# Kernel tuning notes

Measured on AMD Instinct MI355X. Metric: run time of the kernel, lower is better.

## Reference

```python
import jax, jax.numpy as jnp
import numpy as np

B, S, T = 16, 64, 64
H, V = 512, 32000


def _gru_step(h, x_t, W_ih, W_hh, b_ih, b_hh):
    # PyTorch GRU cell: gates ordered (r, z, n)
    gi = x_t @ W_ih.T + b_ih          # [B, 3H]
    gh = h @ W_hh.T + b_hh            # [B, 3H]
    i_r, i_z, i_n = jnp.split(gi, 3, axis=-1)
    h_r, h_z, h_n = jnp.split(gh, 3, axis=-1)
    r = jax.nn.sigmoid(i_r + h_r)
    z = jax.nn.sigmoid(i_z + h_z)
    n = jnp.tanh(i_n + r * h_n)
    return (1.0 - z) * n + z * h


def setup_inputs() -> dict:
    key = jax.random.key(0)
    ks = jax.random.split(key, 16)
    sc = 1.0 / np.sqrt(H)
    d = {
        'x': jax.random.randint(ks[0], (B, S), 0, V),
        'y': jax.random.randint(ks[1], (B, T), 0, V),
        'emb_enc': jax.random.normal(ks[2], (V, H), jnp.float32) * 0.02,
        'W_ih_e': jax.random.normal(ks[3], (3 * H, H), jnp.float32) * sc,
        'W_hh_e': jax.random.normal(ks[4], (3 * H, H), jnp.float32) * sc,
        'b_ih_e': jnp.zeros((3 * H,), jnp.float32),
        'b_hh_e': jnp.zeros((3 * H,), jnp.float32),
        'emb_dec': jax.random.normal(ks[5], (V, H), jnp.float32) * 0.02,
        'W_ih_d': jax.random.normal(ks[6], (3 * H, H), jnp.float32) * sc,
        'W_hh_d': jax.random.normal(ks[7], (3 * H, H), jnp.float32) * sc,
        'b_ih_d': jnp.zeros((3 * H,), jnp.float32),
        'b_hh_d': jnp.zeros((3 * H,), jnp.float32),
        'W_c': jax.random.normal(ks[8], (H, 2 * H), jnp.float32) * sc,
        'b_c': jnp.zeros((H,), jnp.float32),
        'W_out': jax.random.normal(ks[9], (V, H), jnp.float32) * sc,
        'b_out': jnp.zeros((V,), jnp.float32),
    }
    return d


def _forward(x, y, emb_enc, W_ih_e, W_hh_e, b_ih_e, b_hh_e,
             emb_dec, W_ih_d, W_hh_d, b_ih_d, b_hh_d,
             W_c, b_c, W_out, b_out):
    # ---- Encoder: GRU over source tokens (dropout=0 / eval) ----
    emb_x = emb_enc[x]                         # [B, S, H]
    def enc_step(h, e_t):
        h = _gru_step(h, e_t, W_ih_e, W_hh_e, b_ih_e, b_hh_e)
        return h, h
    h0 = jnp.zeros((x.shape[0], H), jnp.float32)
    h_enc, enc_seq = jax.lax.scan(enc_step, h0, jnp.swapaxes(emb_x, 0, 1))
    enc_out = jnp.swapaxes(enc_seq, 0, 1)      # [B, S, H]

    # ---- Decoder: teacher forcing (ratio=1.0), dot-product attention ----
    def dec_step(h, tok):
        e = emb_dec[tok]                                   # [B, H]
        h = _gru_step(h, e, W_ih_d, W_hh_d, b_ih_d, b_hh_d)
        score = jnp.einsum('bh,bsh->bs', h, enc_out)       # dot-product, unscaled
        w = jax.nn.softmax(score, axis=-1)
        attn = jnp.einsum('bs,bsh->bh', w, enc_out)        # [B, H]
        d = jnp.tanh(jnp.concatenate([h, attn], axis=-1) @ W_c.T + b_c)
        logits = d @ W_out.T + b_out                       # [B, V]
        return h, logits
    # decode steps use y[:, 0 .. T-2] as inputs, predict positions 1..T-1
    _, logits_seq = jax.lax.scan(dec_step, h_enc, jnp.swapaxes(y[:, :-1], 0, 1))
    logit = jnp.swapaxes(logits_seq, 0, 1)     # [B, T-1, V]

    tgt = y[:, 1:]
    logp = jax.nn.log_softmax(logit, axis=-1)
    nll = -jnp.take_along_axis(logp, tgt[..., None], axis=-1)[..., 0]
    loss = jnp.mean(nll)
    return logit, loss


def reference(x, y, emb_enc, W_ih_e, W_hh_e, b_ih_e, b_hh_e,
              emb_dec, W_ih_d, W_hh_d, b_ih_d, b_hh_d,
              W_c, b_c, W_out, b_out):
    return _forward(x, y, emb_enc, W_ih_e, W_hh_e, b_ih_e, b_hh_e,
                    emb_dec, W_ih_d, W_hh_d, b_ih_d, b_hh_d,
                    W_c, b_c, W_out, b_out)
```

## Files before the change

kernel.cpp:

```cpp
#include <hip/hip_runtime.h>

typedef unsigned short u16;
typedef unsigned int u32;
typedef __attribute__((ext_vector_type(8))) short short8;
typedef __attribute__((ext_vector_type(4))) float floatx4;

#define B_ 16
#define S_ 64
#define H_ 512
#define V_ 32000
#define G3 1536
#define TD 63
#define MROWS 1008
#define NBLK 16

__device__ __forceinline__ float b2f(u16 u) {
  union { u32 i; float f; } c; c.i = ((u32)u) << 16; return c.f;
}
__device__ __forceinline__ u16 f2b(float f) {
  union { float f; u32 i; } c; c.f = f;
  u32 u = c.i;
  return (u16)((u + 0x7FFFu + ((u >> 16) & 1u)) >> 16);
}
__device__ __forceinline__ short8 pack8(float4 a, float4 b) {
  short8 r;
  r[0] = (short)f2b(a.x); r[1] = (short)f2b(a.y); r[2] = (short)f2b(a.z); r[3] = (short)f2b(a.w);
  r[4] = (short)f2b(b.x); r[5] = (short)f2b(b.y); r[6] = (short)f2b(b.z); r[7] = (short)f2b(b.w);
  return r;
}

__global__ void __launch_bounds__(256) gather_kernel(
    const int* __restrict__ x, const int* __restrict__ y,
    const float* __restrict__ emb_enc, const float* __restrict__ emb_dec,
    u16* __restrict__ ex, u16* __restrict__ ey)
{
  const int r = blockIdx.x, tid = threadIdx.x;
  if (r < B_ * S_) {
    int tok = x[r];
    float2 v = ((const float2*)(emb_enc + (size_t)tok * H_))[tid];
    ((u32*)(ex + (size_t)r * H_))[tid] = (u32)f2b(v.x) | ((u32)f2b(v.y) << 16);
  } else {
    int m = r - B_ * S_;
    int t = m >> 4, b = m & 15;
    int tok = y[b * 64 + t];
    float2 v = ((const float2*)(emb_dec + (size_t)tok * H_))[tid];
    ((u32*)(ey + (size_t)m * H_))[tid] = (u32)f2b(v.x) | ((u32)f2b(v.y) << 16);
  }
}

template <int MODE, int SWAP = 0>
__global__ void __launch_bounds__(256) gemm_bt(
    const u16* __restrict__ A, const float* __restrict__ Bm,
    const float* __restrict__ bias, void* __restrict__ Cout, int M, int N, int K)
{
  __shared__ u16 As[64 * 40];
  __shared__ u16 Bs[128 * 40];
  const int tid = threadIdx.x;
  const int wave = tid >> 6, lane = tid & 63;
  const int l15 = lane & 15, quad = lane >> 4;
  const int m0 = (SWAP ? blockIdx.x : blockIdx.y) * 64;
  const int n0 = (SWAP ? blockIdx.y : blockIdx.x) * 128;
  floatx4 acc[4][2] = {};

  for (int kk = 0; kk < K; kk += 32) {
    {
      int row = tid >> 2, ch = tid & 3;
      short8 v = {};
      int gm = m0 + row;
      if (gm < M) v = *(const short8*)(A + (size_t)gm * K + kk + ch * 8);
      *(short8*)(As + row * 40 + ch * 8) = v;
    }
#pragma unroll
    for (int i = 0; i < 4; ++i) {
      int idx = tid + i * 256;
      int row = idx >> 3, c4 = idx & 7;
      int gn = n0 + row;
      float4 w = *(const float4*)(Bm + (size_t)gn * K + kk + c4 * 4);
      uint2 p;
      p.x = (u32)f2b(w.x) | ((u32)f2b(w.y) << 16);
      p.y = (u32)f2b(w.z) | ((u32)f2b(w.w) << 16);
      *(uint2*)(Bs + row * 40 + c4 * 4) = p;
    }
    __syncthreads();
    short8 af[4], bfr[2];
#pragma unroll
    for (int mt = 0; mt < 4; ++mt)
      af[mt] = *(const short8*)(As + (mt * 16 + l15) * 40 + quad * 8);
#pragma unroll
    for (int nt = 0; nt < 2; ++nt)
      bfr[nt] = *(const short8*)(Bs + (wave * 32 + nt * 16 + l15) * 40 + quad * 8);
#pragma unroll
    for (int mt = 0; mt < 4; ++mt)
#pragma unroll
      for (int nt = 0; nt < 2; ++nt)
        acc[mt][nt] = __builtin_amdgcn_mfma_f32_16x16x32_bf16(af[mt], bfr[nt], acc[mt][nt], 0, 0, 0);
    __syncthreads();
  }
#pragma unroll
  for (int mt = 0; mt < 4; ++mt) {
#pragma unroll
    for (int nt = 0; nt < 2; ++nt) {
      int gn = n0 + wave * 32 + nt * 16 + l15;
      float bv = bias[gn];
#pragma unroll
      for (int r = 0; r < 4; ++r) {
        int gm = m0 + mt * 16 + quad * 4 + r;
        if (gm < M) {
          float v = acc[mt][nt][r] + bv;
          if (MODE == 0) {
            ((float*)Cout)[(size_t)gm * N + gn] = v;
          } else if (MODE == 1) {
            int tt = gm >> 4, bb = gm & 15;
            ((float*)Cout)[((size_t)bb * TD + tt) * V_ + gn] = v;
          } else {
            ((u16*)Cout)[(size_t)gm * N + gn] = f2b(tanhf(v));
          }
        }
      }
    }
  }
}

struct RecArgs {
  const float* gi_enc;
  const float* gi_dec;
  const float* Whe;
  const float* Whd;
  const float* bhe;
  const float* bhd;
  u16* eo;
  u16* ha;
  u16* hcat;
  int* bar;
};

__device__ __forceinline__ void gridbar(int* slots, int gen) {
  __syncthreads();
  if (threadIdx.x < 16) {
    if (threadIdx.x == 0) {
      __builtin_amdgcn_fence(__ATOMIC_RELEASE, "agent");
      __hip_atomic_store(slots + (int)blockIdx.x * 32, gen, __ATOMIC_RELAXED, __HIP_MEMORY_SCOPE_AGENT);
    }
    while (__hip_atomic_load(slots + (int)threadIdx.x * 32, __ATOMIC_RELAXED, __HIP_MEMORY_SCOPE_AGENT) < gen) {}
    __builtin_amdgcn_fence(__ATOMIC_ACQUIRE, "agent");
  }
  __syncthreads();
}

template <int ISENC>
__device__ __forceinline__ void gate_phase(const RecArgs& a, int wave, int l15, int quad,
    int J, int step, int p, const short8* wf, float bh, float* hreg,
    float (&lds_rz)[2][2][16][16])
{
  const int sub = wave % 3, half = wave / 3;
  const int jc = J + half * 16 + l15;
  const float* gi = ISENC ? a.gi_enc : a.gi_dec;
  float giv[4];
#pragma unroll
  for (int r = 0; r < 4; ++r) {
    const int b = quad * 4 + r;
    const int row = ISENC ? (b * 64 + step) : (step * 16 + b);
    giv[r] = gi[(size_t)row * G3 + sub * 512 + jc];
  }
  const u16* hb = a.ha + p * 8192 + l15 * 512 + quad * 8;
  short8 af[16];
#pragma unroll
  for (int kk = 0; kk < 16; ++kk) af[kk] = *(const short8*)(hb + kk * 32);
  floatx4 acc = {0.f, 0.f, 0.f, 0.f};
#pragma unroll
  for (int kk = 0; kk < 16; ++kk)
    acc = __builtin_amdgcn_mfma_f32_16x16x32_bf16(af[kk], wf[(ISENC ? 0 : 16) + kk], acc, 0, 0, 0);
  if (sub < 2) {
#pragma unroll
    for (int r = 0; r < 4; ++r)
      lds_rz[sub][half][quad * 4 + r][l15] = acc[r] + bh + giv[r];
    __syncthreads();
  } else {
    __syncthreads();
    const int pn = p ^ 1;
#pragma unroll
    for (int r = 0; r < 4; ++r) {
      const int b = quad * 4 + r;
      const float rp = lds_rz[0][half][b][l15];
      const float zp = lds_rz[1][half][b][l15];
      const float rr = 1.f / (1.f + __expf(-rp));
      const float zz = 1.f / (1.f + __expf(-zp));
      const float nn = tanhf(giv[r] + rr * (acc[r] + bh));
      const float hv = (1.f - zz) * nn + zz * hreg[r];
      hreg[r] = hv;
      const u16 h16 = f2b(hv);
      a.ha[pn * 8192 + b * 512 + jc] = h16;
      if (ISENC) a.eo[((size_t)(b * 64 + step)) * 512 + jc] = h16;
      else       a.hcat[((size_t)(step * 16 + b)) * 1024 + jc] = h16;
    }
  }
}

__global__ void __launch_bounds__(384) rec_kernel(RecArgs a) {
  __shared__ float lds_rz[2][2][16][16];
  const int tid = threadIdx.x;
  const int wave = tid >> 6, lane = tid & 63;
  const int l15 = lane & 15, quad = lane >> 4;
  const int J = blockIdx.x * 32;
  const int sub = wave % 3, half = wave / 3;

  short8 wf[32];
  const int row = sub * 512 + J + half * 16 + l15;
  const float* pe = a.Whe + (size_t)row * 512 + quad * 8;
  const float* pd = a.Whd + (size_t)row * 512 + quad * 8;
#pragma unroll
  for (int kk = 0; kk < 16; ++kk) {
    wf[kk]      = pack8(*(const float4*)(pe + kk * 32), *(const float4*)(pe + kk * 32 + 4));
    wf[16 + kk] = pack8(*(const float4*)(pd + kk * 32), *(const float4*)(pd + kk * 32 + 4));
  }
  const int jc = J + half * 16 + l15;
  const float bhe = a.bhe[sub * 512 + jc];
  const float bhd = a.bhd[sub * 512 + jc];

  float hreg[4] = {0.f, 0.f, 0.f, 0.f};
  if (sub == 2) {
#pragma unroll
    for (int r = 0; r < 4; ++r)
      a.ha[(quad * 4 + r) * 512 + jc] = 0;
  }
  int gen = 0;
  gridbar(a.bar, ++gen);

  for (int s = 0; s < S_; ++s) {
    gate_phase<1>(a, wave, l15, quad, J, s, s & 1, wf, bhe, hreg, lds_rz);
    gridbar(a.bar, ++gen);
  }

  for (int t = 0; t < TD; ++t) {
    gate_phase<0>(a, wave, l15, quad, J, t, t & 1, wf, bhd, hreg, lds_rz);
    if (t < TD - 1) gridbar(a.bar, ++gen);
  }
}

__global__ void __launch_bounds__(512) attn_kernel(
    const u16* __restrict__ eo16, u16* __restrict__ hcat)
{
  __shared__ float sc[64][9];
  __shared__ float wts[64];
  const int m = blockIdx.x, b = m & 15;
  const int tid = threadIdx.x;
  const u16* eo = eo16 + (size_t)b * 64 * 512;
  const u16* h = hcat + (size_t)m * 1024;
  {
    const int s = tid >> 3, q = tid & 7;
    const u16* ep = eo + s * 512 + q * 64;
    const u16* hp = h + q * 64;
    float acc = 0.f;
#pragma unroll
    for (int u = 0; u < 8; ++u) {
      short8 e8 = *(const short8*)(ep + u * 8);
      short8 h8 = *(const short8*)(hp + u * 8);
#pragma unroll
      for (int i = 0; i < 8; ++i) acc += b2f((u16)e8[i]) * b2f((u16)h8[i]);
    }
    sc[s][q] = acc;
  }
  __syncthreads();
  if (tid < 64) {
    float v = 0.f;
#pragma unroll
    for (int u = 0; u < 8; ++u) v += sc[tid][u];
    float mx = v;
#pragma unroll
    for (int d = 1; d < 64; d <<= 1) mx = fmaxf(mx, __shfl_xor(mx, d));
    float e = __expf(v - mx);
    float sum = e;
#pragma unroll
    for (int d = 1; d < 64; d <<= 1) sum += __shfl_xor(sum, d);
    wts[tid] = e / sum;
  }
  __syncthreads();
  {
    const int j = tid;
    float acc = 0.f;
#pragma unroll 8
    for (int s2 = 0; s2 < 64; ++s2) acc += wts[s2] * b2f(eo[s2 * 512 + j]);
    hcat[(size_t)m * 1024 + 512 + j] = f2b(acc);
  }
}

__global__ void __launch_bounds__(256) loss_rows_kernel(
    const float* __restrict__ logits, const int* __restrict__ y, float* __restrict__ nll)
{
  __shared__ float wm[4], ws_[4];
  const int m = blockIdx.x;
  const int t = m >> 4, b = m & 15;
  const float* row = logits + ((size_t)b * TD + t) * V_;
  const int tid = threadIdx.x;
  const int lane = tid & 63, wave = tid >> 6;

  float mx = -1e30f, sum = 0.f;
  for (int c = tid; c < 8000; c += 256) {
    float4 v = ((const float4*)row)[c];
    float m4 = fmaxf(fmaxf(v.x, v.y), fmaxf(v.z, v.w));
    if (m4 > mx) { sum *= __expf(mx - m4); mx = m4; }
    sum += __expf(v.x - mx) + __expf(v.y - mx) + __expf(v.z - mx) + __expf(v.w - mx);
  }
#pragma unroll
  for (int d = 1; d < 64; d <<= 1) {
    float om = __shfl_xor(mx, d), os = __shfl_xor(sum, d);
    float nm = fmaxf(mx, om);
    sum = sum * __expf(mx - nm) + os * __expf(om - nm);
    mx = nm;
  }
  if (lane == 0) { wm[wave] = mx; ws_[wave] = sum; }
  __syncthreads();
  if (tid == 0) {
    float M = wm[0], S = ws_[0];
#pragma unroll
    for (int u = 1; u < 4; ++u) {
      float nm = fmaxf(M, wm[u]);
      S = S * __expf(M - nm) + ws_[u] * __expf(wm[u] - nm);
      M = nm;
    }
    int tok = y[b * 64 + t + 1];
    nll[m] = M + logf(S) - row[tok];
  }
}

__global__ void __launch_bounds__(256) loss_final_kernel(const float* __restrict__ nll, float* __restrict__ out) {
  __shared__ float wred[4];
  const int tid = threadIdx.x;
  float s = 0.f;
  for (int i = tid; i < MROWS; i += 256) s += nll[i];
#pragma unroll
  for (int d = 1; d < 64; d <<= 1) s += __shfl_xor(s, d);
  if ((tid & 63) == 0) wred[tid >> 6] = s;
  __syncthreads();
  if (tid == 0) out[0] = (wred[0] + wred[1] + wred[2] + wred[3]) / 1008.f;
}

extern "C" void kernel_launch(void* const* d_in, const int* in_sizes, int n_in,
                              void* d_out, int out_size, void* d_ws, size_t ws_size,
                              hipStream_t stream)
{
  const int*   x       = (const int*)d_in[0];
  const int*   y       = (const int*)d_in[1];
  const float* emb_enc = (const float*)d_in[2];
  const float* W_ih_e  = (const float*)d_in[3];
  const float* W_hh_e  = (const float*)d_in[4];
  const float* b_ih_e  = (const float*)d_in[5];
  const float* b_hh_e  = (const float*)d_in[6];
  const float* emb_dec = (const float*)d_in[7];
  const float* W_ih_d  = (const float*)d_in[8];
  const float* W_hh_d  = (const float*)d_in[9];
  const float* b_ih_d  = (const float*)d_in[10];
  const float* b_hh_d  = (const float*)d_in[11];
  const float* W_c     = (const float*)d_in[12];
  const float* b_c     = (const float*)d_in[13];
  const float* W_out   = (const float*)d_in[14];
  const float* b_out   = (const float*)d_in[15];

  char* ws = (char*)d_ws;
  float* gi_enc = (float*)(ws + 0);
  float* gi_dec = (float*)(ws + 6291456);
  u16* embx     = (u16*)(ws + 12484608);
  u16* emby     = (u16*)(ws + 13533184);
  u16* hcat     = (u16*)(ws + 12484608);
  u16* Dm       = (u16*)(ws + 14565376);
  u16* eo16     = (u16*)(ws + 15597568);
  u16* ha16     = (u16*)(ws + 16646144);
  float* nll    = (float*)(ws + 16678912);
  int* bar      = (int*)(ws + 16682944);

  hipMemsetAsync(bar, 0, 2048, stream);

  gather_kernel<<<dim3(B_ * S_ + MROWS), dim3(256), 0, stream>>>(x, y, emb_enc, emb_dec, embx, emby);

  gemm_bt<0><<<dim3(12, 16), dim3(256), 0, stream>>>(embx, W_ih_e, b_ih_e, (void*)gi_enc, 1024, G3, 512);
  gemm_bt<0><<<dim3(12, 16), dim3(256), 0, stream>>>(emby, W_ih_d, b_ih_d, (void*)gi_dec, MROWS, G3, 512);

  RecArgs ra{gi_enc, gi_dec, W_hh_e, W_hh_d, b_hh_e, b_hh_d, eo16, ha16, hcat, bar};
  rec_kernel<<<dim3(NBLK), dim3(384), 0, stream>>>(ra);

  attn_kernel<<<dim3(MROWS), dim3(512), 0, stream>>>(eo16, hcat);

  gemm_bt<2><<<dim3(4, 16), dim3(256), 0, stream>>>(hcat, W_c, b_c, (void*)Dm, MROWS, 512, 1024);

  gemm_bt<1, 1><<<dim3(16, 250), dim3(256), 0, stream>>>(Dm, W_out, b_out, d_out, MROWS, V_, 512);
  loss_rows_kernel<<<dim3(MROWS), dim3(256), 0, stream>>>((const float*)d_out, y, nll);
  loss_final_kernel<<<dim3(1), dim3(256), 0, stream>>>(nll, ((float*)d_out) + (size_t)MROWS * V_);
}
```

Baseline: 1.188 ms.

## Fuse embedding gather into GEMMs and partial softmax into output projection

The embedding gather is folded into the input-projection GEMM's A-tile load, which removes the separate gather kernel and its bf16 staging buffers. The vocabulary GEMM epilogue now computes per-tile row max and sum-exp partials and captures the target logit, so a small merge kernel replaces the second full pass over the 1008x32000 logits. The recurrent kernel also prefetches the next step's input-gate values before the grid barrier and writes hidden states as packed 32-bit pairs. The cost is more epilogue work and an extra partials buffer, which reuses the gi_enc workspace region after the recurrence has finished.

```diff
diff --git a/kernel.cpp b/kernel.cpp
--- a/kernel.cpp
+++ b/kernel.cpp
@@ -13,6 +13,7 @@
 #define TD 63
 #define MROWS 1008
 #define NBLK 16
+#define NTILES 250
 
 __device__ __forceinline__ float b2f(u16 u) {
   union { u32 i; float f; } c; c.i = ((u32)u) << 16; return c.f;
@@ -29,29 +30,12 @@
   return r;
 }
 
-__global__ void __launch_bounds__(256) gather_kernel(
-    const int* __restrict__ x, const int* __restrict__ y,
-    const float* __restrict__ emb_enc, const float* __restrict__ emb_dec,
-    u16* __restrict__ ex, u16* __restrict__ ey)
-{
-  const int r = blockIdx.x, tid = threadIdx.x;
-  if (r < B_ * S_) {
-    int tok = x[r];
-    float2 v = ((const float2*)(emb_enc + (size_t)tok * H_))[tid];
-    ((u32*)(ex + (size_t)r * H_))[tid] = (u32)f2b(v.x) | ((u32)f2b(v.y) << 16);
-  } else {
-    int m = r - B_ * S_;
-    int t = m >> 4, b = m & 15;
-    int tok = y[b * 64 + t];
-    float2 v = ((const float2*)(emb_dec + (size_t)tok * H_))[tid];
-    ((u32*)(ey + (size_t)m * H_))[tid] = (u32)f2b(v.x) | ((u32)f2b(v.y) << 16);
-  }
-}
-
-template <int MODE, int SWAP = 0>
+template <int MODE, int SWAP = 0, int GATHER = 0>
 __global__ void __launch_bounds__(256) gemm_bt(
-    const u16* __restrict__ A, const float* __restrict__ Bm,
-    const float* __restrict__ bias, void* __restrict__ Cout, int M, int N, int K)
+    const u16* __restrict__ A, const float* __restrict__ Aemb,
+    const int* __restrict__ idx, const float* __restrict__ Bm,
+    const float* __restrict__ bias, void* __restrict__ Cout, int M, int N, int K,
+    float* __restrict__ prtl, float* __restrict__ tokv, const int* __restrict__ yarr)
 {
   __shared__ u16 As[64 * 40];
   __shared__ u16 Bs[128 * 40];
@@ -67,13 +51,21 @@
       int row = tid >> 2, ch = tid & 3;
       short8 v = {};
       int gm = m0 + row;
-      if (gm < M) v = *(const short8*)(A + (size_t)gm * K + kk + ch * 8);
+      if (gm < M) {
+        if (GATHER == 0) {
+          v = *(const short8*)(A + (size_t)gm * K + kk + ch * 8);
+        } else {
+          int tok = (GATHER == 1) ? idx[gm] : idx[((gm & 15) << 6) + (gm >> 4)];
+          const float* src = Aemb + (size_t)tok * 512 + kk + ch * 8;
+          v = pack8(*(const float4*)src, *(const float4*)(src + 4));
+        }
+      }
       *(short8*)(As + row * 40 + ch * 8) = v;
     }
 #pragma unroll
     for (int i = 0; i < 4; ++i) {
-      int idx = tid + i * 256;
-      int row = idx >> 3, c4 = idx & 7;
+      int idx2 = tid + i * 256;
+      int row = idx2 >> 3, c4 = idx2 & 7;
       int gn = n0 + row;
       float4 w = *(const float4*)(Bm + (size_t)gn * K + kk + c4 * 4);
       uint2 p;
@@ -96,24 +88,68 @@
         acc[mt][nt] = __builtin_amdgcn_mfma_f32_16x16x32_bf16(af[mt], bfr[nt], acc[mt][nt], 0, 0, 0);
     __syncthreads();
   }
-#pragma unroll
-  for (int mt = 0; mt < 4; ++mt) {
-#pragma unroll
-    for (int nt = 0; nt < 2; ++nt) {
-      int gn = n0 + wave * 32 + nt * 16 + l15;
-      float bv = bias[gn];
+
+  if (MODE == 1) {
+    __shared__ float2 red[4][64];
+    const int y0 = n0 >> 7;
+#pragma unroll
+    for (int mt = 0; mt < 4; ++mt) {
 #pragma unroll
       for (int r = 0; r < 4; ++r) {
-        int gm = m0 + mt * 16 + quad * 4 + r;
+        const int gm = m0 + mt * 16 + quad * 4 + r;
+        const int gn0 = n0 + wave * 32 + l15;
+        float vv0 = acc[mt][0][r] + bias[gn0];
+        float vv1 = acc[mt][1][r] + bias[gn0 + 16];
         if (gm < M) {
-          float v = acc[mt][nt][r] + bv;
-          if (MODE == 0) {
-            ((float*)Cout)[(size_t)gm * N + gn] = v;
-          } else if (MODE == 1) {
-            int tt = gm >> 4, bb = gm & 15;
-            ((float*)Cout)[((size_t)bb * TD + tt) * V_ + gn] = v;
-          } else {
-            ((u16*)Cout)[(size_t)gm * N + gn] = f2b(tanhf(v));
+          const int tt = gm >> 4, bb = gm & 15;
+          float* orow = (float*)Cout + ((size_t)bb * TD + tt) * V_;
+          orow[gn0] = vv0;
+          orow[gn0 + 16] = vv1;
+          const int tok = yarr[bb * 64 + tt + 1];
+          if (tok == gn0) tokv[gm] = vv0;
+          if (tok == gn0 + 16) tokv[gm] = vv1;
+        }
+        float mx = fmaxf(vv0, vv1);
+        float sm = __expf(vv0 - mx) + __expf(vv1 - mx);
+#pragma unroll
+        for (int d = 1; d < 16; d <<= 1) {
+          const float om = __shfl_xor(mx, d), os = __shfl_xor(sm, d);
+          const float nm = fmaxf(mx, om);
+          sm = sm * __expf(mx - nm) + os * __expf(om - nm);
+          mx = nm;
+        }
+        if (l15 == 0) red[wave][mt * 16 + quad * 4 + r] = make_float2(mx, sm);
+      }
+    }
+    __syncthreads();
+    if (tid < 64) {
+      const float2 p0 = red[0][tid], p1 = red[1][tid], p2 = red[2][tid], p3 = red[3][tid];
+      float M2 = fmaxf(fmaxf(p0.x, p1.x), fmaxf(p2.x, p3.x));
+      float S2 = p0.y * __expf(p0.x - M2) + p1.y * __expf(p1.x - M2)
+               + p2.y * __expf(p2.x - M2) + p3.y * __expf(p3.x - M2);
+      const int gm = m0 + tid;
+      if (gm < M) {
+        float* pp = prtl + ((size_t)gm * NTILES + y0) * 2;
+        pp[0] = M2; pp[1] = S2;
+      }
+    }
+  } else {
+#pragma unroll
+    for (int mt = 0; mt < 4; ++mt) {
+#pragma unroll
+      for (int nt = 0; nt < 2; ++nt) {
+        int gn = n0 + wave * 32 + nt * 16 + l15;
+        float bv = bias[gn];
+#pragma unroll
+        for (int r = 0; r < 4; ++r) {
+          int gm = m0 + mt * 16 + quad * 4 + r;
+          if (gm < M) {
+            float v = acc[mt][nt][r] + bv;
+            if (MODE == 0) {
+              ((float*)Cout)[(size_t)gm * N + gn] = v;
+            } else {
+              ((u16*)Cout)[(size_t)gm * N + gn] = f2b(tanhf(v));
+            }
           }
         }
       }
@@ -148,20 +184,12 @@
 }
 
 template <int ISENC>
-__device__ __forceinline__ void gate_phase(const RecArgs& a, int wave, int l15, int quad,
-    int J, int step, int p, const short8* wf, float bh, float* hreg,
+__device__ __forceinline__ void gate_phase(const RecArgs& a, int wave, int lane, int l15, int quad,
+    int J, int step, int p, const short8* wf, float bh, float* hreg, const float* giv,
     float (&lds_rz)[2][2][16][16])
 {
   const int sub = wave % 3, half = wave / 3;
   const int jc = J + half * 16 + l15;
-  const float* gi = ISENC ? a.gi_enc : a.gi_dec;
-  float giv[4];
-#pragma unroll
-  for (int r = 0; r < 4; ++r) {
-    const int b = quad * 4 + r;
-    const int row = ISENC ? (b * 64 + step) : (step * 16 + b);
-    giv[r] = gi[(size_t)row * G3 + sub * 512 + jc];
-  }
   const u16* hb = a.ha + p * 8192 + l15 * 512 + quad * 8;
   short8 af[16];
 #pragma unroll
@@ -189,9 +217,12 @@
       const float hv = (1.f - zz) * nn + zz * hreg[r];
       hreg[r] = hv;
       const u16 h16 = f2b(hv);
-      a.ha[pn * 8192 + b * 512 + jc] = h16;
-      if (ISENC) a.eo[((size_t)(b * 64 + step)) * 512 + jc] = h16;
-      else       a.hcat[((size_t)(step * 16 + b)) * 1024 + jc] = h16;
+      const u32 up = (u32)h16 | ((u32)(u16)__shfl_xor((int)h16, 1) << 16);
+      if (!(lane & 1)) {
+        *(u32*)(a.ha + pn * 8192 + b * 512 + jc) = up;
+        if (ISENC) *(u32*)(a.eo + ((size_t)(b * 64 + step)) * 512 + jc) = up;
+        else       *(u32*)(a.hcat + ((size_t)(step * 16 + b)) * 1024 + jc) = up;
+      }
     }
   }
 }
@@ -218,22 +249,41 @@
   const float bhd = a.bhd[sub * 512 + jc];
 
   float hreg[4] = {0.f, 0.f, 0.f, 0.f};
-  if (sub == 2) {
+  float giv[4];
+#pragma unroll
+  for (int r = 0; r < 4; ++r)
+    giv[r] = a.gi_enc[(size_t)((quad * 4 + r) * 64) * G3 + sub * 512 + jc];
+
+  if (sub == 2 && !(lane & 1)) {
 #pragma unroll
     for (int r = 0; r < 4; ++r)
-      a.ha[(quad * 4 + r) * 512 + jc] = 0;
+      *(u32*)(a.ha + (quad * 4 + r) * 512 + jc) = 0u;
   }
   int gen = 0;
   gridbar(a.bar, ++gen);
 
   for (int s = 0; s < S_; ++s) {
-    gate_phase<1>(a, wave, l15, quad, J, s, s & 1, wf, bhe, hreg, lds_rz);
+    gate_phase<1>(a, wave, lane, l15, quad, J, s, s & 1, wf, bhe, hreg, giv, lds_rz);
+    if (s < S_ - 1) {
+#pragma unroll
+      for (int r = 0; r < 4; ++r)
+        giv[r] = a.gi_enc[((size_t)((quad * 4 + r) * 64 + s + 1)) * G3 + sub * 512 + jc];
+    } else {
+#pragma unroll
+      for (int r = 0; r < 4; ++r)
+        giv[r] = a.gi_dec[((size_t)(quad * 4 + r)) * G3 + sub * 512 + jc];
+    }
     gridbar(a.bar, ++gen);
   }
 
   for (int t = 0; t < TD; ++t) {
-    gate_phase<0>(a, wave, l15, quad, J, t, t & 1, wf, bhd, hreg, lds_rz);
-    if (t < TD - 1) gridbar(a.bar, ++gen);
+    gate_phase<0>(a, wave, lane, l15, quad, J, t, t & 1, wf, bhd, hreg, giv, lds_rz);
+    if (t < TD - 1) {
+#pragma unroll
+      for (int r = 0; r < 4; ++r)
+        giv[r] = a.gi_dec[((size_t)((t + 1) * 16 + quad * 4 + r)) * G3 + sub * 512 + jc];
+      gridbar(a.bar, ++gen);
+    }
   }
 }
 
@@ -284,43 +334,27 @@
   }
 }
 
-__global__ void __launch_bounds__(256) loss_rows_kernel(
-    const float* __restrict__ logits, const int* __restrict__ y, float* __restrict__ nll)
+__global__ void __launch_bounds__(64) loss_merge_kernel(
+    const float* __restrict__ prtl, const float* __restrict__ tokv, float* __restrict__ nll)
 {
-  __shared__ float wm[4], ws_[4];
   const int m = blockIdx.x;
-  const int t = m >> 4, b = m & 15;
-  const float* row = logits + ((size_t)b * TD + t) * V_;
-  const int tid = threadIdx.x;
-  const int lane = tid & 63, wave = tid >> 6;
-
-  float mx = -1e30f, sum = 0.f;
-  for (int c = tid; c < 8000; c += 256) {
-    float4 v = ((const float4*)row)[c];
-    float m4 = fmaxf(fmaxf(v.x, v.y), fmaxf(v.z, v.w));
-    if (m4 > mx) { sum *= __expf(mx - m4); mx = m4; }
-    sum += __expf(v.x - mx) + __expf(v.y - mx) + __expf(v.z - mx) + __expf(v.w - mx);
+  const int lane = threadIdx.x;
+  float mx = -1e30f, sm = 0.f;
+  for (int i = lane; i < NTILES; i += 64) {
+    const float pm = prtl[((size_t)m * NTILES + i) * 2];
+    const float ps = prtl[((size_t)m * NTILES + i) * 2 + 1];
+    const float nm = fmaxf(mx, pm);
+    sm = sm * __expf(mx - nm) + ps * __expf(pm - nm);
+    mx = nm;
   }
 #pragma unroll
   for (int d = 1; d < 64; d <<= 1) {
-    float om = __shfl_xor(mx, d), os = __shfl_xor(sum, d);
-    float nm = fmaxf(mx, om);
-    sum = sum * __expf(mx - nm) + os * __expf(om - nm);
+    const float om = __shfl_xor(mx, d), os = __shfl_xor(sm, d);
+    const float nm = fmaxf(mx, om);
+    sm = sm * __expf(mx - nm) + os * __expf(om - nm);
     mx = nm;
   }
-  if (lane == 0) { wm[wave] = mx; ws_[wave] = sum; }
-  __syncthreads();
-  if (tid == 0) {
-    float M = wm[0], S = ws_[0];
-#pragma unroll
-    for (int u = 1; u < 4; ++u) {
-      float nm = fmaxf(M, wm[u]);
-      S = S * __expf(M - nm) + ws_[u] * __expf(wm[u] - nm);
-      M = nm;
-    }
-    int tok = y[b * 64 + t + 1];
-    nll[m] = M + logf(S) - row[tok];
-  }
+  if (lane == 0) nll[m] = mx + logf(sm) - tokv[m];
 }
 
 __global__ void __launch_bounds__(256) loss_final_kernel(const float* __restrict__ nll, float* __restrict__ out) {
@@ -359,30 +393,33 @@
   char* ws = (char*)d_ws;
   float* gi_enc = (float*)(ws + 0);
   float* gi_dec = (float*)(ws + 6291456);
-  u16* embx     = (u16*)(ws + 12484608);
-  u16* emby     = (u16*)(ws + 13533184);
   u16* hcat     = (u16*)(ws + 12484608);
   u16* Dm       = (u16*)(ws + 14565376);
   u16* eo16     = (u16*)(ws + 15597568);
   u16* ha16     = (u16*)(ws + 16646144);
   float* nll    = (float*)(ws + 16678912);
   int* bar      = (int*)(ws + 16682944);
+  float* prtl   = (float*)(ws + 0);
+  float* tokv   = (float*)(ws + 2016000);
 
   hipMemsetAsync(bar, 0, 2048, stream);
 
-  gather_kernel<<<dim3(B_ * S_ + MROWS), dim3(256), 0, stream>>>(x, y, emb_enc, emb_dec, embx, emby);
-
-  gemm_bt<0><<<dim3(12, 16), dim3(256), 0, stream>>>(embx, W_ih_e, b_ih_e, (void*)gi_enc, 1024, G3, 512);
-  gemm_bt<0><<<dim3(12, 16), dim3(256), 0, stream>>>(emby, W_ih_d, b_ih_d, (void*)gi_dec, MROWS, G3, 512);
+  gemm_bt<0, 0, 1><<<dim3(12, 16), dim3(256), 0, stream>>>(
+      nullptr, emb_enc, x, W_ih_e, b_ih_e, (void*)gi_enc, 1024, G3, 512, nullptr, nullptr, nullptr);
+  gemm_bt<0, 0, 2><<<dim3(12, 16), dim3(256), 0, stream>>>(
+      nullptr, emb_dec, y, W_ih_d, b_ih_d, (void*)gi_dec, MROWS, G3, 512, nullptr, nullptr, nullptr);
 
   RecArgs ra{gi_enc, gi_dec, W_hh_e, W_hh_d, b_hh_e, b_hh_d, eo16, ha16, hcat, bar};
   rec_kernel<<<dim3(NBLK), dim3(384), 0, stream>>>(ra);
 
   attn_kernel<<<dim3(MROWS), dim3(512), 0, stream>>>(eo16, hcat);
 
-  gemm_bt<2><<<dim3(4, 16), dim3(256), 0, stream>>>(hcat, W_c, b_c, (void*)Dm, MROWS, 512, 1024);
-
-  gemm_bt<1, 1><<<dim3(16, 250), dim3(256), 0, stream>>>(Dm, W_out, b_out, d_out, MROWS, V_, 512);
-  loss_rows_kernel<<<dim3(MROWS), dim3(256), 0, stream>>>((const float*)d_out, y, nll);
+  gemm_bt<2><<<dim3(4, 16), dim3(256), 0, stream>>>(
+      hcat, nullptr, nullptr, W_c, b_c, (void*)Dm, MROWS, 512, 1024, nullptr, nullptr, nullptr);
+
+  gemm_bt<1, 1><<<dim3(16, NTILES), dim3(256), 0, stream>>>(
+      Dm, nullptr, nullptr, W_out, b_out, d_out, MROWS, V_, 512, prtl, tokv, y);
+
+  loss_merge_kernel<<<dim3(MROWS), dim3(64), 0, stream>>>(prtl, tokv, nll);
   loss_final_kernel<<<dim3(1), dim3(256), 0, stream>>>(nll, ((float*)d_out) + (size_t)MROWS * V_);
 }
```

Measured after the change: 1.339 ms. +12.7%, slower.

## Replace GRU grid barrier with per-wave flag polling over a step arena

Applied to the files above, without the earlier changes.

Swaps the full grid barrier between recurrent steps for per-half-block flags that the producing wave sets after its hidden-state stores drain. Consumer lanes poll the 32 flags directly before reading the next step's state. The hidden state is no longer ping-ponged between two buffers: each step gets its own slot in an arena placed in the output buffer (zeroed first, later overwritten by the logits), so no step can overwrite state another block is still reading. Stores are packed into 32-bit atomics. The aim is to cut per-step barrier latency across 127 sequential steps, at the cost of relaxed-ordering subtleties and reliance on the output buffer as scratch.

```diff
diff --git a/kernel.cpp b/kernel.cpp
--- a/kernel.cpp
+++ b/kernel.cpp
@@ -72,8 +72,8 @@
     }
 #pragma unroll
     for (int i = 0; i < 4; ++i) {
-      int idx = tid + i * 256;
-      int row = idx >> 3, c4 = idx & 7;
+      int idx2 = tid + i * 256;
+      int row = idx2 >> 3, c4 = idx2 & 7;
       int gn = n0 + row;
       float4 w = *(const float4*)(Bm + (size_t)gn * K + kk + c4 * 4);
       uint2 p;
@@ -129,28 +129,22 @@
   const float* bhe;
   const float* bhd;
   u16* eo;
-  u16* ha;
+  u16* arena;
   u16* hcat;
   int* bar;
 };
 
-__device__ __forceinline__ void gridbar(int* slots, int gen) {
-  __syncthreads();
-  if (threadIdx.x < 16) {
-    if (threadIdx.x == 0) {
-      __builtin_amdgcn_fence(__ATOMIC_RELEASE, "agent");
-      __hip_atomic_store(slots + (int)blockIdx.x * 32, gen, __ATOMIC_RELAXED, __HIP_MEMORY_SCOPE_AGENT);
-    }
-    while (__hip_atomic_load(slots + (int)threadIdx.x * 32, __ATOMIC_RELAXED, __HIP_MEMORY_SCOPE_AGENT) < gen) {}
-    __builtin_amdgcn_fence(__ATOMIC_ACQUIRE, "agent");
-  }
-  __syncthreads();
+__device__ __forceinline__ void pollbar(const int* slots, int lane, int gen) {
+  if (gen > 0) {
+    while (__hip_atomic_load(slots + (lane & 31) * 32, __ATOMIC_RELAXED, __HIP_MEMORY_SCOPE_AGENT) < gen) {}
+  }
+  asm volatile("" ::: "memory");
 }
 
 template <int ISENC>
-__device__ __forceinline__ void gate_phase(const RecArgs& a, int wave, int l15, int quad,
-    int J, int step, int p, const short8* wf, float bh, float* hreg,
-    float (&lds_rz)[2][2][16][16])
+__device__ __forceinline__ void gate_phase(const RecArgs& a, int wave, int lane, int l15, int quad,
+    int J, int step, int astep, const short8* wf, float bh, float* hreg,
+    float (&lds_rz)[2][2][16][16], bool do_signal)
 {
   const int sub = wave % 3, half = wave / 3;
   const int jc = J + half * 16 + l15;
@@ -162,7 +156,7 @@
     const int row = ISENC ? (b * 64 + step) : (step * 16 + b);
     giv[r] = gi[(size_t)row * G3 + sub * 512 + jc];
   }
-  const u16* hb = a.ha + p * 8192 + l15 * 512 + quad * 8;
+  const u16* hb = a.arena + (size_t)astep * 8192 + l15 * 512 + quad * 8;
   short8 af[16];
 #pragma unroll
   for (int kk = 0; kk < 16; ++kk) af[kk] = *(const short8*)(hb + kk * 32);
@@ -177,7 +171,6 @@
     __syncthreads();
   } else {
     __syncthreads();
-    const int pn = p ^ 1;
 #pragma unroll
     for (int r = 0; r < 4; ++r) {
       const int b = quad * 4 + r;
@@ -189,9 +182,19 @@
       const float hv = (1.f - zz) * nn + zz * hreg[r];
       hreg[r] = hv;
       const u16 h16 = f2b(hv);
-      a.ha[pn * 8192 + b * 512 + jc] = h16;
-      if (ISENC) a.eo[((size_t)(b * 64 + step)) * 512 + jc] = h16;
-      else       a.hcat[((size_t)(step * 16 + b)) * 1024 + jc] = h16;
+      const u32 up = (u32)h16 | ((u32)(u16)__shfl_xor((int)h16, 1) << 16);
+      if (!(lane & 1)) {
+        __hip_atomic_store((u32*)(a.arena + (size_t)(astep + 1) * 8192 + b * 512 + jc), up,
+                           __ATOMIC_RELAXED, __HIP_MEMORY_SCOPE_AGENT);
+        if (ISENC) *(u32*)(a.eo + ((size_t)(b * 64 + step)) * 512 + jc) = up;
+        else       *(u32*)(a.hcat + ((size_t)(step * 16 + b)) * 1024 + jc) = up;
+      }
+    }
+    if (do_signal) {
+      asm volatile("s_waitcnt vmcnt(0)" ::: "memory");
+      if (lane == 0)
+        __hip_atomic_store(a.bar + ((int)blockIdx.x * 2 + half) * 32, astep + 1,
+                           __ATOMIC_RELAXED, __HIP_MEMORY_SCOPE_AGENT);
     }
   }
 }
@@ -218,22 +221,15 @@
   const float bhd = a.bhd[sub * 512 + jc];
 
   float hreg[4] = {0.f, 0.f, 0.f, 0.f};
-  if (sub == 2) {
-#pragma unroll
-    for (int r = 0; r < 4; ++r)
-      a.ha[(quad * 4 + r) * 512 + jc] = 0;
-  }
-  int gen = 0;
-  gridbar(a.bar, ++gen);
+
 
   for (int s = 0; s < S_; ++s) {
-    gate_phase<1>(a, wave, l15, quad, J, s, s & 1, wf, bhe, hreg, lds_rz);
-    gridbar(a.bar, ++gen);
-  }
-
+    pollbar(a.bar, lane, s);
+    gate_phase<1>(a, wave, lane, l15, quad, J, s, s, wf, bhe, hreg, lds_rz, true);
+  }
   for (int t = 0; t < TD; ++t) {
-    gate_phase<0>(a, wave, l15, quad, J, t, t & 1, wf, bhd, hreg, lds_rz);
-    if (t < TD - 1) gridbar(a.bar, ++gen);
+    pollbar(a.bar, lane, 64 + t);
+    gate_phase<0>(a, wave, lane, l15, quad, J, t, 64 + t, wf, bhd, hreg, lds_rz, t < TD - 1);
   }
 }
 
@@ -364,18 +360,20 @@
   u16* hcat     = (u16*)(ws + 12484608);
   u16* Dm       = (u16*)(ws + 14565376);
   u16* eo16     = (u16*)(ws + 15597568);
-  u16* ha16     = (u16*)(ws + 16646144);
   float* nll    = (float*)(ws + 16678912);
   int* bar      = (int*)(ws + 16682944);
 
-  hipMemsetAsync(bar, 0, 2048, stream);
+  u16* arena = (u16*)d_out;
+
+  hipMemsetAsync(bar, 0, 4096, stream);
+  hipMemsetAsync(d_out, 0, 16384, stream);
 
   gather_kernel<<<dim3(B_ * S_ + MROWS), dim3(256), 0, stream>>>(x, y, emb_enc, emb_dec, embx, emby);
 
   gemm_bt<0><<<dim3(12, 16), dim3(256), 0, stream>>>(embx, W_ih_e, b_ih_e, (void*)gi_enc, 1024, G3, 512);
   gemm_bt<0><<<dim3(12, 16), dim3(256), 0, stream>>>(emby, W_ih_d, b_ih_d, (void*)gi_dec, MROWS, G3, 512);
 
-  RecArgs ra{gi_enc, gi_dec, W_hh_e, W_hh_d, b_hh_e, b_hh_d, eo16, ha16, hcat, bar};
+  RecArgs ra{gi_enc, gi_dec, W_hh_e, W_hh_d, b_hh_e, b_hh_d, eo16, arena, hcat, bar};
   rec_kernel<<<dim3(NBLK), dim3(384), 0, stream>>>(ra);
 
   attn_kernel<<<dim3(MROWS), dim3(512), 0, stream>>>(eo16, hcat);
```

Result: slower. 1.280 ms (+7.7%).

## Stage recurrent outputs in LDS and remap output GEMM blocks across XCDs

Applied to the files above, without the earlier changes.

The recurrent kernel now keeps each step's encoder outputs and decoder hidden states in a large dynamic LDS buffer, packs pairs of bf16 values via lane shuffles into 32-bit stores, and writes them to global memory only after the loop. This removes scattered 2-byte global stores from the latency-bound per-step critical path. The vocabulary GEMM switches to a 1D grid with an XCD-aware block mapping, so the M-tiles that share a W_out column panel land on the same XCD for L2 reuse. Costs are about 130KB of LDS per block and padded blocks that exit early.

```diff
diff --git a/kernel.cpp b/kernel.cpp
--- a/kernel.cpp
+++ b/kernel.cpp
@@ -13,6 +13,8 @@
 #define TD 63
 #define MROWS 1008
 #define NBLK 16
+
+#define REC_LDS_BYTES (4096 + 65536 + 64512)
 
 __device__ __forceinline__ float b2f(u16 u) {
   union { u32 i; float f; } c; c.i = ((u32)u) << 16; return c.f;
@@ -58,8 +60,17 @@
   const int tid = threadIdx.x;
   const int wave = tid >> 6, lane = tid & 63;
   const int l15 = lane & 15, quad = lane >> 4;
-  const int m0 = (SWAP ? blockIdx.x : blockIdx.y) * 64;
-  const int n0 = (SWAP ? blockIdx.y : blockIdx.x) * 128;
+  int m0, n0;
+  if (SWAP == 2) {
+    const int bid = blockIdx.x;
+    const int xcd = bid & 7, w = bid >> 3;
+    const int mt = w & 15, ph = w >> 4;
+    const int p = ph * 8 + xcd;
+    if (p >= N / 128) return;
+    m0 = mt * 64; n0 = p * 128;
+  } else {
+    m0 = blockIdx.y * 64; n0 = blockIdx.x * 128;
+  }
   floatx4 acc[4][2] = {};
 
   for (int kk = 0; kk < K; kk += 32) {
@@ -72,8 +83,8 @@
     }
 #pragma unroll
     for (int i = 0; i < 4; ++i) {
-      int idx = tid + i * 256;
-      int row = idx >> 3, c4 = idx & 7;
+      int idx2 = tid + i * 256;
+      int row = idx2 >> 3, c4 = idx2 & 7;
       int gn = n0 + row;
       float4 w = *(const float4*)(Bm + (size_t)gn * K + kk + c4 * 4);
       uint2 p;
@@ -147,10 +158,12 @@
   __syncthreads();
 }
 
+typedef float rz_t[2][16][16];
+
 template <int ISENC>
-__device__ __forceinline__ void gate_phase(const RecArgs& a, int wave, int l15, int quad,
+__device__ __forceinline__ void gate_phase(const RecArgs& a, int wave, int lane, int l15, int quad,
     int J, int step, int p, const short8* wf, float bh, float* hreg,
-    float (&lds_rz)[2][2][16][16])
+    rz_t* lds_rz, u32* eoL, u32* hcL)
 {
   const int sub = wave % 3, half = wave / 3;
   const int jc = J + half * 16 + l15;
@@ -189,15 +202,23 @@
       const float hv = (1.f - zz) * nn + zz * hreg[r];
       hreg[r] = hv;
       const u16 h16 = f2b(hv);
-      a.ha[pn * 8192 + b * 512 + jc] = h16;
-      if (ISENC) a.eo[((size_t)(b * 64 + step)) * 512 + jc] = h16;
-      else       a.hcat[((size_t)(step * 16 + b)) * 1024 + jc] = h16;
+      const u32 up = (u32)h16 | ((u32)(u16)__shfl_xor((int)h16, 1) << 16);
+      if (!(lane & 1)) {
+        *(u32*)(a.ha + pn * 8192 + b * 512 + jc) = up;
+        const int c2 = half * 8 + (l15 >> 1);
+        if (ISENC) eoL[(b * 64 + step) * 16 + c2] = up;
+        else       hcL[(step * 16 + b) * 16 + c2] = up;
+      }
     }
   }
 }
 
 __global__ void __launch_bounds__(384) rec_kernel(RecArgs a) {
-  __shared__ float lds_rz[2][2][16][16];
+  extern __shared__ char smem[];
+  rz_t* lds_rz = (rz_t*)smem;
+  u32* eoL = (u32*)(smem + 4096);
+  u32* hcL = (u32*)(smem + 4096 + 65536);
+
   const int tid = threadIdx.x;
   const int wave = tid >> 6, lane = tid & 63;
   const int l15 = lane & 15, quad = lane >> 4;
@@ -227,13 +248,22 @@
   gridbar(a.bar, ++gen);
 
   for (int s = 0; s < S_; ++s) {
-    gate_phase<1>(a, wave, l15, quad, J, s, s & 1, wf, bhe, hreg, lds_rz);
+    gate_phase<1>(a, wave, lane, l15, quad, J, s, s & 1, wf, bhe, hreg, lds_rz, eoL, hcL);
     gridbar(a.bar, ++gen);
   }
-
   for (int t = 0; t < TD; ++t) {
-    gate_phase<0>(a, wave, l15, quad, J, t, t & 1, wf, bhd, hreg, lds_rz);
+    gate_phase<0>(a, wave, lane, l15, quad, J, t, t & 1, wf, bhd, hreg, lds_rz, eoL, hcL);
     if (t < TD - 1) gridbar(a.bar, ++gen);
+  }
+
+  __syncthreads();
+  for (int i = tid; i < 16 * 64 * 16; i += 384) {
+    const int c2 = i & 15, rs = i >> 4;
+    *(u32*)(a.eo + (size_t)rs * 512 + J + c2 * 2) = eoL[i];
+  }
+  for (int i = tid; i < 63 * 16 * 16; i += 384) {
+    const int c2 = i & 15, rt = i >> 4;
+    *(u32*)(a.hcat + (size_t)rt * 1024 + J + c2 * 2) = hcL[i];
   }
 }
 
@@ -370,19 +400,26 @@
 
   hipMemsetAsync(bar, 0, 2048, stream);
 
+  static bool attr_set = false;
+  if (!attr_set) {
+    hipFuncSetAttribute((const void*)rec_kernel,
+                        hipFuncAttributeMaxDynamicSharedMemorySize, REC_LDS_BYTES);
+    attr_set = true;
+  }
+
   gather_kernel<<<dim3(B_ * S_ + MROWS), dim3(256), 0, stream>>>(x, y, emb_enc, emb_dec, embx, emby);
 
   gemm_bt<0><<<dim3(12, 16), dim3(256), 0, stream>>>(embx, W_ih_e, b_ih_e, (void*)gi_enc, 1024, G3, 512);
   gemm_bt<0><<<dim3(12, 16), dim3(256), 0, stream>>>(emby, W_ih_d, b_ih_d, (void*)gi_dec, MROWS, G3, 512);
 
   RecArgs ra{gi_enc, gi_dec, W_hh_e, W_hh_d, b_hh_e, b_hh_d, eo16, ha16, hcat, bar};
-  rec_kernel<<<dim3(NBLK), dim3(384), 0, stream>>>(ra);
+  rec_kernel<<<dim3(NBLK), dim3(384), REC_LDS_BYTES, stream>>>(ra);
 
   attn_kernel<<<dim3(MROWS), dim3(512), 0, stream>>>(eo16, hcat);
 
   gemm_bt<2><<<dim3(4, 16), dim3(256), 0, stream>>>(hcat, W_c, b_c, (void*)Dm, MROWS, 512, 1024);
 
-  gemm_bt<1, 1><<<dim3(16, 250), dim3(256), 0, stream>>>(Dm, W_out, b_out, d_out, MROWS, V_, 512);
+  gemm_bt<1, 2><<<dim3(4096), dim3(256), 0, stream>>>(Dm, W_out, b_out, d_out, MROWS, V_, 512);
   loss_rows_kernel<<<dim3(MROWS), dim3(256), 0, stream>>>((const float*)d_out, y, nll);
   loss_final_kernel<<<dim3(1), dim3(256), 0, stream>>>(nll, ((float*)d_out) + (size_t)MROWS * V_);
 }
```

After: 1.187 ms. Within noise of the previous version (-0.1%).
